# Kernel optimization log

Measured on AMD Instinct MI355X. Metric: run time of the kernel, lower is better.

The kernel has to match this reference:

```python
import jax, jax.numpy as jnp
import numpy as np

B, D, H, W, L = 32, 768, 14, 14, 77
TEMP_G, TEMP1, TEMP2, TEMP3 = 10.0, 4.0, 5.0, 10.0
LAMBDA_G, LAMBDA_L = 1.0, 1.0
EPS = 1e-8
NEG = -1e30


def setup_inputs() -> dict:
    key = jax.random.key(0)
    k1, k2, k3, k4, k5 = jax.random.split(key, 5)
    img_global = jax.random.normal(k1, (B, D), dtype=jnp.float32)
    img_local = jax.random.normal(k2, (B, D, H, W), dtype=jnp.float32)
    text_global = jax.random.normal(k3, (B, D), dtype=jnp.float32)
    text_local = jax.random.normal(k4, (B, L, D), dtype=jnp.float32)
    # ragged caption lengths: prefix attention mask, lengths in [10, L]
    lens = jax.random.randint(k5, (B,), 10, L + 1)
    attention_mask = (jnp.arange(L)[None, :] < lens[:, None]).astype(jnp.int32)
    return {"img_global": img_global, "img_local": img_local,
            "text_global": text_global, "text_local": text_local,
            "attention_mask": attention_mask}


def _ce_arange(scores):
    # cross entropy with labels = arange(n), mean reduction
    return jnp.mean(jax.nn.logsumexp(scores, axis=1) - jnp.diagonal(scores))


def _gloria_loss(img_global, img_local, text_global, text_local, attention_mask):
    mask = attention_mask.astype(bool)                      # [B, L]
    # ---- global contrastive loss ----
    in_ = img_global / jnp.maximum(jnp.linalg.norm(img_global, axis=1, keepdims=True), 1e-12)
    tn_ = text_global / jnp.maximum(jnp.linalg.norm(text_global, axis=1, keepdims=True), 1e-12)
    g_scores = (in_ @ tn_.T) * TEMP_G                       # [B, B]
    loss_global = 0.5 * (_ce_arange(g_scores) + _ce_arange(g_scores.T))

    # ---- local contrastive loss (vectorized over all text/image pairs) ----
    tl = jnp.swapaxes(text_local, 1, 2)                     # [B, D, L] (forward() transposes since L != D)
    ctx = img_local.reshape(B, D, H * W)                    # [B, D, S]
    # raw attention logits: text i words vs image j pixels -> [i, j, s, l]
    logits = jnp.einsum('jds,idl->ijsl', ctx, tl)
    logits = jnp.where(mask[:, None, None, :], logits, NEG)
    a1 = jax.nn.softmax(logits, axis=-1)                    # softmax over words (first softmax)
    a2 = jax.nn.softmax(TEMP1 * jnp.swapaxes(a1, 2, 3), axis=-1)  # [i, j, l, s], softmax over pixels
    wctx = jnp.einsum('jds,ijls->ijdl', ctx, a2)            # weighted context [i, j, D, l]
    # cosine similarity per word, over feature dim
    w12 = jnp.einsum('idl,ijdl->ijl', tl, wctx)
    n1 = jnp.linalg.norm(tl, axis=1)                        # [i, l]
    n2 = jnp.linalg.norm(wctx, axis=2)                      # [i, j, l]
    cos = w12 / jnp.maximum(n1[:, None, :] * n2, EPS)       # [i, j, l]
    row = jnp.exp(TEMP2 * cos) * mask[:, None, :]           # mask padded words
    sim = jnp.log(row.sum(axis=-1))                         # [i, j]  (local_agg='sum')
    # torch cats per-caption columns: similarities[j, i] -> transpose
    scores = sim.T * TEMP3                                  # [img j, text i]
    loss_local = 0.5 * (_ce_arange(scores) + _ce_arange(scores.T))

    return LAMBDA_G * loss_global + LAMBDA_L * loss_local


def reference(img_global, img_local, text_global, text_local, attention_mask):
    return _gloria_loss(img_global, img_local, text_global, text_local, attention_mask)
```

## Files before the change

### kernel.cpp

```cpp
#include <hip/hip_runtime.h>
#include <math.h>

#define NB 32
#define ND 768
#define NS 196
#define NL 77

typedef _Float16 f16x8 __attribute__((ext_vector_type(8)));
typedef float f32x4 __attribute__((ext_vector_type(4)));

__device__ __forceinline__ f32x4 mfma16(f16x8 a, f16x8 b, f32x4 c) {
  return __builtin_amdgcn_mfma_f32_16x16x32_f16(a, b, c, 0, 0, 0);
}

#define GLOAD16(gp, lp)                                          \
  __builtin_amdgcn_global_load_lds(                              \
      (const __attribute__((address_space(1))) void*)(gp),       \
      (__attribute__((address_space(3))) void*)(lp), 16, 0, 0)


__global__ __launch_bounds__(256) void prep_all_kernel(
    const float* __restrict__ text_local,
    const float* __restrict__ img_local,
    const int* __restrict__ amask,
    _Float16* __restrict__ txf, _Float16* __restrict__ cTf,
    float* __restrict__ n1ws, int* __restrict__ lenws) {
  const int bid = blockIdx.x;
  const int t = threadIdx.x;
  __shared__ float tile[32][213];

  if (bid < 960) {
    int tau = bid * 256 + t;
    int i = tau / 7680;
    int r = tau - i * 7680;
    int dk = r / 320;
    int r2 = r - dk * 320;
    int lt = r2 >> 6, lane = r2 & 63;
    int n16 = lane & 15, g = lane >> 4;
    int l = lt * 16 + n16;
    float v[8];
#pragma unroll
    for (int q = 0; q < 8; ++q) v[q] = 0.f;
    if (l < NL) {
      const float* src = text_local + ((size_t)i * NL + l) * ND + dk * 32 + g * 8;
      float4 a = *(const float4*)src;
      float4 b = *(const float4*)(src + 4);
      v[0] = a.x; v[1] = a.y; v[2] = a.z; v[3] = a.w;
      v[4] = b.x; v[5] = b.y; v[6] = b.z; v[7] = b.w;
    }
    f16x8 hv;
#pragma unroll
    for (int q = 0; q < 8; ++q) hv[q] = (_Float16)v[q];
    size_t base = (((size_t)i * 24 + dk) * 5 + lt) * 512 + (size_t)lane * 8;
    *(f16x8*)(txf + base) = hv;
  } else if (bid < 1344) {
    const int b2 = bid - 960;
    const int j = b2 / 12, dc = b2 - (b2 / 12) * 12;
    const float* src = img_local + ((size_t)j * ND + dc * 64) * NS;
#pragma unroll 1
    for (int h = 0; h < 2; ++h) {
      __syncthreads();
      for (int idx = t; idx < 1568; idx += 256) {
        int dd = idx / 49, sq = idx - dd * 49;
        float4 v = *(const float4*)(src + (size_t)(h * 32 + dd) * NS + sq * 4);
        tile[dd][sq * 4 + 0] = v.x;
        tile[dd][sq * 4 + 1] = v.y;
        tile[dd][sq * 4 + 2] = v.z;
        tile[dd][sq * 4 + 3] = v.w;
      }
      __syncthreads();
      const int dk = dc * 2 + h;
      for (int idx = t; idx < 832; idx += 256) {
        int lane = idx & 63;
        int S = idx >> 6;
        int n16 = lane & 15, g = lane >> 4;
        int s = S * 16 + n16;
        f16x8 hv;
#pragma unroll
        for (int e = 0; e < 8; ++e) {
          float v = (s < NS) ? tile[g * 8 + e][s] : 0.f;
          hv[e] = (_Float16)v;
        }
        size_t base = (((size_t)j * 13 + S) * 24 + dk) * 512 + (size_t)lane * 8;
        *(f16x8*)(cTf + base) = hv;
      }
    }
  } else {
    const int i = bid - 1344;
    const int lane = t & 63, w = t >> 6;
    __shared__ int slen;
    if (t == 0) slen = 0;
    __syncthreads();
    if (t < NL && amask[i * NL + t] != 0) atomicAdd(&slen, 1);
    for (int l = w; l < NL; l += 4) {
      const float4* p = (const float4*)(text_local + ((size_t)i * NL + l) * ND);
      float s = 0.f;
#pragma unroll
      for (int k = 0; k < 3; ++k) {
        float4 v = p[lane + 64 * k];
        s += v.x * v.x + v.y * v.y + v.z * v.z + v.w * v.w;
      }
#pragma unroll
      for (int off = 32; off; off >>= 1) s += __shfl_xor(s, off);
      if (lane == 0) n1ws[i * 80 + l] = sqrtf(s);
    }
    __syncthreads();
    if (t == 0) lenws[i] = slen;
  }
}

__global__ void mid_kernel(const _Float16* __restrict__ cTf, _Float16* __restrict__ Gf,
                           const float* __restrict__ img_global,
                           const float* __restrict__ text_global,
                           float* __restrict__ gscw,
                           const int* __restrict__ lenws, int* __restrict__ ordws) {
  const int bid = blockIdx.x;
  const int t = threadIdx.x;
  __shared__ __align__(16) float shi[ND];

  if (bid < 832) {
    const int j = bid / 26;
    const int rr = bid - j * 26;
    const int st = rr >> 1, ch = rr & 1;
    const int lane = t & 63, w = t >> 6;
    const int g = lane >> 4, n16 = lane & 15;
    const f32x4 z4 = {0.f, 0.f, 0.f, 0.f};
    f32x4 accG[2];
    accG[0] = z4; accG[1] = z4;
    const int base = ch * 7;
    const int ncols = ch ? 6 : 7;
    const size_t cj = (size_t)j * 13;
    for (int dk = 0; dk < 24; ++dk) {
      size_t ao = ((cj + st) * 24 + dk) * 512 + (size_t)lane * 8;
      f16x8 A = *(const f16x8*)(cTf + ao);
#pragma unroll
      for (int q = 0; q < 2; ++q) {
        int ntl = w + (q << 2);
        if (ntl < ncols) {
          int nt = base + ntl;
          size_t bo = ((cj + nt) * 24 + dk) * 512 + (size_t)lane * 8;
          f16x8 B = *(const f16x8*)(cTf + bo);
          accG[q] = mfma16(A, B, accG[q]);
        }
      }
    }
#pragma unroll
    for (int q = 0; q < 2; ++q) {
      int ntl = w + (q << 2);
      int nt = base + ntl;
      bool compute = (ntl < ncols);
      bool zfill = (ch == 1 && nt == 13);
      if (compute || zfill) {
#pragma unroll
        for (int r = 0; r < 4; ++r) {
          int col = nt * 16 + n16;
          float v = compute ? accG[q][r] : 0.f;
          int kt = col >> 5, gg = (col >> 3) & 3, e = col & 7;
          int lane2 = (g * 4 + r) + (gg << 4);
          size_t o = (((size_t)j * 13 + st) * 7 + kt) * 512 + (size_t)lane2 * 8 + e;
          Gf[o] = (_Float16)v;
        }
      }
    }
  } else if (bid < 864) {
    const int a = bid - 832;
    const int lane = t & 63, w = t >> 6;
    if (t < ND / 4) ((float4*)shi)[t] = ((const float4*)(img_global + (size_t)a * ND))[t];
    __syncthreads();
    for (int b = w; b < NB; b += 4) {
      const float4* pt = (const float4*)(text_global + (size_t)b * ND);
      const float4* pi = (const float4*)shi;
      float dot = 0.f, ni = 0.f, nt = 0.f;
#pragma unroll
      for (int k = 0; k < 3; ++k) {
        float4 x = pi[lane + 64 * k];
        float4 y = pt[lane + 64 * k];
        dot += x.x * y.x + x.y * y.y + x.z * y.z + x.w * y.w;
        ni  += x.x * x.x + x.y * x.y + x.z * x.z + x.w * x.w;
        nt  += y.x * y.x + y.y * y.y + y.z * y.z + y.w * y.w;
      }
#pragma unroll
      for (int off = 32; off; off >>= 1) {
        dot += __shfl_xor(dot, off);
        ni  += __shfl_xor(ni, off);
        nt  += __shfl_xor(nt, off);
      }
      if (lane == 0)
        gscw[a * NB + b] = dot / fmaxf(sqrtf(ni), 1e-12f) / fmaxf(sqrtf(nt), 1e-12f) * 10.0f;
    }
  } else {
    if (t == 0) {
      int o[32];
      for (int k = 0; k < 32; ++k) o[k] = k;
      for (int x = 0; x < 31; ++x) {
        int best = x;
        for (int y = x + 1; y < 32; ++y)
          if (lenws[o[y]] > lenws[o[best]]) best = y;
        int tmp = o[x]; o[x] = o[best]; o[best] = tmp;
      }
      for (int k = 0; k < 32; ++k) ordws[k] = o[k];
    }
  }
}

__global__ __launch_bounds__(512, 3) void pair_kernel(
    const _Float16* __restrict__ txf, const _Float16* __restrict__ cTf,
    const _Float16* __restrict__ Gf,
    const float* __restrict__ n1ws, const int* __restrict__ lenws,
    const int* __restrict__ ordws,
    float* __restrict__ simws) {
  const int t = threadIdx.x;
  const int wg = ((blockIdx.x & 7) << 6) + (blockIdx.x >> 3);
  const int j = wg >> 4;
  const int m = wg & 15;
  const int i0 = ordws[m], i1 = ordws[31 - m];
  const int len0 = lenws[i0], len1 = lenws[i1];
  const int nlt0 = (len0 + 15) >> 4, nlt1 = (len1 + 15) >> 4;
  const int lane = t & 63, wid = t >> 6;
  const int g = lane >> 4, n16 = lane & 15;
  const bool vb = (wid < 5);

  __shared__ __align__(16) union {
    _Float16 e2f[7 * 5 * 64 * 8];
    _Float16 b1[2][2][5][512];
  } U;
  __shared__ float w12s[80], z2s[80], n2s[80];

  const f32x4 z4 = {0.f, 0.f, 0.f, 0.f};
  f32x4 acc[2][2][5];
#pragma unroll
  for (int p = 0; p < 2; ++p)
#pragma unroll
    for (int q = 0; q < 2; ++q)
#pragma unroll
      for (int lt = 0; lt < 5; ++lt) acc[p][q][lt] = z4;

  const _Float16* txi0 = txf + (size_t)i0 * 24 * 5 * 512;
  const _Float16* txi1 = txf + (size_t)i1 * 24 * 5 * 512;
  const size_t cj = (size_t)j * 13;
  const int c0 = (wid < 5) ? wid : (wid - 5);

  GLOAD16(txi0 + ((size_t)c0 << 9) + ((size_t)lane << 3), &U.b1[0][0][c0][0]);
  GLOAD16(txi1 + ((size_t)c0 << 9) + ((size_t)lane << 3), &U.b1[0][1][c0][0]);
  __syncthreads();

#pragma unroll 1
  for (int dk = 0; dk < 24; ++dk) {
    const int cur = dk & 1;
    f16x8 Aa, Ab;
    {
      size_t ao = ((cj + wid) * 24 + dk) * 512 + ((size_t)lane << 3);
      Aa = *(const f16x8*)(cTf + ao);
    }
    if (vb) {
      size_t ao = ((cj + wid + 8) * 24 + dk) * 512 + ((size_t)lane << 3);
      Ab = *(const f16x8*)(cTf + ao);
    }
    if (dk < 23) {
      GLOAD16(txi0 + ((size_t)((dk + 1) * 5 + c0) << 9) + ((size_t)lane << 3),
              &U.b1[cur ^ 1][0][c0][0]);
      GLOAD16(txi1 + ((size_t)((dk + 1) * 5 + c0) << 9) + ((size_t)lane << 3),
              &U.b1[cur ^ 1][1][c0][0]);
    }
    __builtin_amdgcn_s_setprio(1);
#pragma unroll
    for (int lt = 0; lt < 5; ++lt) {
      if (lt < nlt0) {
        f16x8 B0 = *(const f16x8*)&U.b1[cur][0][lt][lane << 3];
        acc[0][0][lt] = mfma16(Aa, B0, acc[0][0][lt]);
        if (vb) acc[0][1][lt] = mfma16(Ab, B0, acc[0][1][lt]);
      }
      if (lt < nlt1) {
        f16x8 B1 = *(const f16x8*)&U.b1[cur][1][lt][lane << 3];
        acc[1][0][lt] = mfma16(Aa, B1, acc[1][0][lt]);
        if (vb) acc[1][1][lt] = mfma16(Ab, B1, acc[1][1][lt]);
      }
    }
    __builtin_amdgcn_s_setprio(0);
    __syncthreads();
  }

#pragma unroll
  for (int p = 0; p < 2; ++p) {
    const int ip   = p ? i1 : i0;
    const int lenp = p ? len1 : len0;
    const int nltp = p ? nlt1 : nlt0;

    __syncthreads();
    if (t < 80) { w12s[t] = 0.f; z2s[t] = 0.f; n2s[t] = 0.f; }
    for (int idx = t; idx < 2240; idx += 512)
      ((uint4*)U.e2f)[idx] = make_uint4(0, 0, 0, 0);
    __syncthreads();

    float w12loc[5], z2loc[5];
#pragma unroll
    for (int lt = 0; lt < 5; ++lt) { w12loc[lt] = 0.f; z2loc[lt] = 0.f; }
#pragma unroll
    for (int q = 0; q < 2; ++q) {
      const int S = wid + (q << 3);
      if (q == 0 || vb) {
#pragma unroll
        for (int r = 0; r < 4; ++r) {
          int s = S * 16 + g * 4 + r;
          bool srow = (s < NS);
          float mx = -1e30f;
#pragma unroll
          for (int lt = 0; lt < 5; ++lt) {
            if (lt < nltp) {
              if ((lt * 16 + n16) < lenp) mx = fmaxf(mx, acc[p][q][lt][r]);
            }
          }
          mx = fmaxf(mx, __shfl_xor(mx, 1));
          mx = fmaxf(mx, __shfl_xor(mx, 2));
          mx = fmaxf(mx, __shfl_xor(mx, 4));
          mx = fmaxf(mx, __shfl_xor(mx, 8));
          float z = 0.f;
          float ev[5];
#pragma unroll
          for (int lt = 0; lt < 5; ++lt) {
            float e = 0.f;
            if (lt < nltp) {
              if ((lt * 16 + n16) < lenp) e = __expf(acc[p][q][lt][r] - mx);
            }
            ev[lt] = e;
            z += e;
          }
          z += __shfl_xor(z, 1);
          z += __shfl_xor(z, 2);
          z += __shfl_xor(z, 4);
          z += __shfl_xor(z, 8);
          float inv = 4.0f / z;
#pragma unroll
          for (int lt = 0; lt < 5; ++lt) {
            if (lt < nltp) {
              if (((lt * 16 + n16) < lenp) && srow) {
                float e2 = __expf(ev[lt] * inv);
                w12loc[lt] += e2 * acc[p][q][lt][r];
                z2loc[lt] += e2;
                int kt = s >> 5, kk = s & 31;
                U.e2f[(((kt * 5) + lt) * 64 + (n16 + ((kk >> 3) << 4))) * 8 + (kk & 7)] = (_Float16)e2;
              }
            }
          }
        }
      }
    }
#pragma unroll
    for (int lt = 0; lt < 5; ++lt) {
      w12loc[lt] += __shfl_xor(w12loc[lt], 16);
      w12loc[lt] += __shfl_xor(w12loc[lt], 32);
      z2loc[lt] += __shfl_xor(z2loc[lt], 16);
      z2loc[lt] += __shfl_xor(z2loc[lt], 32);
    }
    if (lane < 16) {
#pragma unroll
      for (int lt = 0; lt < 5; ++lt) {
        if (lt < nltp) {
          atomicAdd(&w12s[lt * 16 + lane], w12loc[lt]);
          atomicAdd(&z2s[lt * 16 + lane], z2loc[lt]);
        }
      }
    }
    __syncthreads();

    float n2loc[5];
#pragma unroll
    for (int lt = 0; lt < 5; ++lt) n2loc[lt] = 0.f;
#pragma unroll
    for (int q = 0; q < 2; ++q) {
      const int S = wid + (q << 3);
      if (q == 0 || vb) {
        f32x4 a2[5];
#pragma unroll
        for (int lt = 0; lt < 5; ++lt) a2[lt] = z4;
        const _Float16* gp = Gf + (((size_t)j * 13 + S) * 7) * 512 + ((size_t)lane << 3);
        f16x8 GA = *(const f16x8*)gp;
#pragma unroll
        for (int kt = 0; kt < 7; ++kt) {
          f16x8 GAN;
          if (kt < 6) GAN = *(const f16x8*)(gp + (size_t)(kt + 1) * 512);
          __builtin_amdgcn_s_setprio(1);
#pragma unroll
          for (int lt = 0; lt < 5; ++lt) {
            if (lt < nltp) {
              f16x8 Bv = *(const f16x8*)&U.e2f[(((kt * 5) + lt) * 64 + lane) * 8];
              a2[lt] = mfma16(GA, Bv, a2[lt]);
            }
          }
          __builtin_amdgcn_s_setprio(0);
          if (kt < 6) GA = GAN;
        }
#pragma unroll
        for (int lt = 0; lt < 5; ++lt) {
          if (lt < nltp) {
#pragma unroll
            for (int r = 0; r < 4; ++r) {
              int s = S * 16 + g * 4 + r;
              int kt = s >> 5, kk = s & 31;
              float e2v = (float)U.e2f[(((kt * 5) + lt) * 64 + (n16 + ((kk >> 3) << 4))) * 8 + (kk & 7)];
              n2loc[lt] += e2v * a2[lt][r];
            }
          }
        }
      }
    }
#pragma unroll
    for (int lt = 0; lt < 5; ++lt) {
      n2loc[lt] += __shfl_xor(n2loc[lt], 16);
      n2loc[lt] += __shfl_xor(n2loc[lt], 32);
    }
    if (lane < 16) {
#pragma unroll
      for (int lt = 0; lt < 5; ++lt) {
        if (lt < nltp) atomicAdd(&n2s[lt * 16 + lane], n2loc[lt]);
      }
    }
    __syncthreads();

    if (t < lenp) {
      float z2 = z2s[t];
      float w12v = w12s[t] / z2;
      float n2v = sqrtf(n2s[t]) / z2;
      float n1v = n1ws[ip * 80 + t];
      float cosv = w12v / fmaxf(n1v * n2v, 1e-8f);
      w12s[t] = __expf(5.0f * cosv);
    }
    __syncthreads();
    if (wid == 0) {
      float e = (lane < lenp) ? w12s[lane] : 0.f;
      if (lane + 64 < lenp) e += w12s[lane + 64];
      e += __shfl_xor(e, 1);
      e += __shfl_xor(e, 2);
      e += __shfl_xor(e, 4);
      e += __shfl_xor(e, 8);
      e += __shfl_xor(e, 16);
      e += __shfl_xor(e, 32);
      if (lane == 0) simws[ip * NB + j] = __logf(e);
    }
  }
}

__global__ void loss_kernel(const float* __restrict__ gscw,
                            const float* __restrict__ simws,
                            float* __restrict__ out) {
  const int t = threadIdx.x;
  __shared__ float gs[NB][NB];
  __shared__ float sl[NB][NB];
  __shared__ float parts[4][NB];
  {
    float4 gv = ((const float4*)gscw)[t];
    ((float4*)gs)[t] = gv;
    float4 v = ((const float4*)simws)[t];
    int ii = t >> 3;
    int j0 = (t & 7) * 4;
    sl[j0 + 0][ii] = v.x * 10.0f;
    sl[j0 + 1][ii] = v.y * 10.0f;
    sl[j0 + 2][ii] = v.z * 10.0f;
    sl[j0 + 3][ii] = v.w * 10.0f;
  }
  __syncthreads();
  if (t < NB) {
    float m, z;
    m = -1e30f;
    for (int c = 0; c < NB; ++c) m = fmaxf(m, gs[t][c]);
    z = 0.f;
    for (int c = 0; c < NB; ++c) z += __expf(gs[t][c] - m);
    parts[0][t] = m + __logf(z) - gs[t][t];

    m = -1e30f;
    for (int c = 0; c < NB; ++c) m = fmaxf(m, gs[c][t]);
    z = 0.f;
    for (int c = 0; c < NB; ++c) z += __expf(gs[c][t] - m);
    parts[1][t] = m + __logf(z) - gs[t][t];

    m = -1e30f;
    for (int c = 0; c < NB; ++c) m = fmaxf(m, sl[t][c]);
    z = 0.f;
    for (int c = 0; c < NB; ++c) z += __expf(sl[t][c] - m);
    parts[2][t] = m + __logf(z) - sl[t][t];

    m = -1e30f;
    for (int c = 0; c < NB; ++c) m = fmaxf(m, sl[c][t]);
    z = 0.f;
    for (int c = 0; c < NB; ++c) z += __expf(sl[c][t] - m);
    parts[3][t] = m + __logf(z) - sl[t][t];
  }
  __syncthreads();
  if (t == 0) {
    float s0 = 0.f, s1 = 0.f, s2 = 0.f, s3 = 0.f;
    for (int r = 0; r < NB; ++r) {
      s0 += parts[0][r]; s1 += parts[1][r];
      s2 += parts[2][r]; s3 += parts[3][r];
    }
    out[0] = 0.5f * (s0 + s1) / 32.0f + 0.5f * (s2 + s3) / 32.0f;
  }
}

extern "C" void kernel_launch(void* const* d_in, const int* in_sizes, int n_in,
                              void* d_out, int out_size, void* d_ws, size_t ws_size,
                              hipStream_t stream) {
  (void)in_sizes; (void)n_in; (void)out_size; (void)ws_size;
  const float* img_global  = (const float*)d_in[0];
  const float* img_local   = (const float*)d_in[1];
  const float* text_global = (const float*)d_in[2];
  const float* text_local  = (const float*)d_in[3];
  const int*   amask       = (const int*)d_in[4];

  _Float16* txf = (_Float16*)d_ws;
  _Float16* cTf = txf + (size_t)1966080;
  _Float16* Gf  = cTf + (size_t)5111808;
  float* fsm  = (float*)(Gf + (size_t)1490944);
  float* n1ws  = fsm;
  float* simws = fsm + 2560;
  float* gscw  = fsm + 3584;
  int*   lenws = (int*)(fsm + 4608);
  int*   ordws = (int*)(fsm + 4640);

  prep_all_kernel<<<1376, 256, 0, stream>>>(text_local, img_local, amask,
                                            txf, cTf, n1ws, lenws);
  mid_kernel<<<865, 256, 0, stream>>>(cTf, Gf, img_global, text_global,
                                      gscw, lenws, ordws);
  pair_kernel<<<512, 512, 0, stream>>>(txf, cTf, Gf, n1ws, lenws, ordws, simws);
  loss_kernel<<<1, 256, 0, stream>>>(gscw, simws, (float*)d_out);
}
```

Measured before the change: 121.9 us.

## Triple-chunk the pair-kernel K loop and fuse the loss kernel via last-block counter

The pair kernel's reduction loop now handles three K-chunks per iteration, loading three A fragments and prefetching three B tiles into a larger LDS double buffer. This cuts barriers and loop overhead by a factor of three. The separate single-block loss kernel is removed: each pair block bumps a global counter after writing its similarity, and the last block to finish computes the cross-entropy loss. This saves one kernel launch but uses more LDS, which may lower occupancy, and relies on atomic and fence ordering for correctness.

```diff
diff --git a/kernel.cpp b/kernel.cpp
--- a/kernel.cpp
+++ b/kernel.cpp
@@ -113,7 +113,8 @@
                            const float* __restrict__ img_global,
                            const float* __restrict__ text_global,
                            float* __restrict__ gscw,
-                           const int* __restrict__ lenws, int* __restrict__ ordws) {
+                           const int* __restrict__ lenws, int* __restrict__ ordws,
+                           unsigned int* __restrict__ donews) {
   const int bid = blockIdx.x;
   const int t = threadIdx.x;
   __shared__ __align__(16) float shi[ND];
@@ -199,6 +200,7 @@
         int tmp = o[x]; o[x] = o[best]; o[best] = tmp;
       }
       for (int k = 0; k < 32; ++k) ordws[k] = o[k];
+      *donews = 0u;
     }
   }
 }
@@ -208,7 +210,8 @@
     const _Float16* __restrict__ Gf,
     const float* __restrict__ n1ws, const int* __restrict__ lenws,
     const int* __restrict__ ordws,
-    float* __restrict__ simws) {
+    float* __restrict__ simws, const float* __restrict__ gscw,
+    unsigned int* __restrict__ donews, float* __restrict__ out) {
   const int t = threadIdx.x;
   const int wg = ((blockIdx.x & 7) << 6) + (blockIdx.x >> 3);
   const int j = wg >> 4;
@@ -222,9 +225,11 @@
 
   __shared__ __align__(16) union {
     _Float16 e2f[7 * 5 * 64 * 8];
-    _Float16 b1[2][2][5][512];
+    _Float16 b1[2][3][2][5][512];
+    struct { float gs[NB][NB]; float sl[NB][NB]; float parts[4][NB]; } loss;
   } U;
   __shared__ float w12s[80], z2s[80], n2s[80];
+  __shared__ int amLast;
 
   const f32x4 z4 = {0.f, 0.f, 0.f, 0.f};
   f32x4 acc[2][2][5];
@@ -240,40 +245,56 @@
   const size_t cj = (size_t)j * 13;
   const int c0 = (wid < 5) ? wid : (wid - 5);
 
-  GLOAD16(txi0 + ((size_t)c0 << 9) + ((size_t)lane << 3), &U.b1[0][0][c0][0]);
-  GLOAD16(txi1 + ((size_t)c0 << 9) + ((size_t)lane << 3), &U.b1[0][1][c0][0]);
+#pragma unroll
+  for (int d = 0; d < 3; ++d) {
+    GLOAD16(txi0 + ((size_t)(d * 5 + c0) << 9) + ((size_t)lane << 3), &U.b1[0][d][0][c0][0]);
+    GLOAD16(txi1 + ((size_t)(d * 5 + c0) << 9) + ((size_t)lane << 3), &U.b1[0][d][1][c0][0]);
+  }
   __syncthreads();
 
 #pragma unroll 1
-  for (int dk = 0; dk < 24; ++dk) {
-    const int cur = dk & 1;
-    f16x8 Aa, Ab;
+  for (int dkp = 0; dkp < 8; ++dkp) {
+    const int cur = dkp & 1;
+    const int dk0 = dkp * 3;
+    f16x8 Aa0, Aa1, Aa2, Ab0, Ab1, Ab2;
     {
-      size_t ao = ((cj + wid) * 24 + dk) * 512 + ((size_t)lane << 3);
-      Aa = *(const f16x8*)(cTf + ao);
+      size_t ao = ((cj + wid) * 24 + dk0) * 512 + ((size_t)lane << 3);
+      Aa0 = *(const f16x8*)(cTf + ao);
+      Aa1 = *(const f16x8*)(cTf + ao + 512);
+      Aa2 = *(const f16x8*)(cTf + ao + 1024);
     }
     if (vb) {
-      size_t ao = ((cj + wid + 8) * 24 + dk) * 512 + ((size_t)lane << 3);
-      Ab = *(const f16x8*)(cTf + ao);
-    }
-    if (dk < 23) {
-      GLOAD16(txi0 + ((size_t)((dk + 1) * 5 + c0) << 9) + ((size_t)lane << 3),
-              &U.b1[cur ^ 1][0][c0][0]);
-      GLOAD16(txi1 + ((size_t)((dk + 1) * 5 + c0) << 9) + ((size_t)lane << 3),
-              &U.b1[cur ^ 1][1][c0][0]);
+      size_t ao = ((cj + wid + 8) * 24 + dk0) * 512 + ((size_t)lane << 3);
+      Ab0 = *(const f16x8*)(cTf + ao);
+      Ab1 = *(const f16x8*)(cTf + ao + 512);
+      Ab2 = *(const f16x8*)(cTf + ao + 1024);
+    }
+    if (dkp < 7) {
+#pragma unroll
+      for (int d = 0; d < 3; ++d) {
+        GLOAD16(txi0 + ((size_t)((dk0 + 3 + d) * 5 + c0) << 9) + ((size_t)lane << 3),
+                &U.b1[cur ^ 1][d][0][c0][0]);
+        GLOAD16(txi1 + ((size_t)((dk0 + 3 + d) * 5 + c0) << 9) + ((size_t)lane << 3),
+                &U.b1[cur ^ 1][d][1][c0][0]);
+      }
     }
     __builtin_amdgcn_s_setprio(1);
 #pragma unroll
-    for (int lt = 0; lt < 5; ++lt) {
-      if (lt < nlt0) {
-        f16x8 B0 = *(const f16x8*)&U.b1[cur][0][lt][lane << 3];
-        acc[0][0][lt] = mfma16(Aa, B0, acc[0][0][lt]);
-        if (vb) acc[0][1][lt] = mfma16(Ab, B0, acc[0][1][lt]);
-      }
-      if (lt < nlt1) {
-        f16x8 B1 = *(const f16x8*)&U.b1[cur][1][lt][lane << 3];
-        acc[1][0][lt] = mfma16(Aa, B1, acc[1][0][lt]);
-        if (vb) acc[1][1][lt] = mfma16(Ab, B1, acc[1][1][lt]);
+    for (int d = 0; d < 3; ++d) {
+      f16x8 Aa = (d == 0) ? Aa0 : (d == 1) ? Aa1 : Aa2;
+      f16x8 Ab = (d == 0) ? Ab0 : (d == 1) ? Ab1 : Ab2;
+#pragma unroll
+      for (int lt = 0; lt < 5; ++lt) {
+        if (lt < nlt0) {
+          f16x8 B0 = *(const f16x8*)&U.b1[cur][d][0][lt][lane << 3];
+          acc[0][0][lt] = mfma16(Aa, B0, acc[0][0][lt]);
+          if (vb) acc[0][1][lt] = mfma16(Ab, B0, acc[0][1][lt]);
+        }
+        if (lt < nlt1) {
+          f16x8 B1 = *(const f16x8*)&U.b1[cur][d][1][lt][lane << 3];
+          acc[1][0][lt] = mfma16(Aa, B1, acc[1][0][lt]);
+          if (vb) acc[1][1][lt] = mfma16(Ab, B1, acc[1][1][lt]);
+        }
       }
     }
     __builtin_amdgcn_s_setprio(0);
@@ -435,62 +456,61 @@
       e += __shfl_xor(e, 8);
       e += __shfl_xor(e, 16);
       e += __shfl_xor(e, 32);
-      if (lane == 0) simws[ip * NB + j] = __logf(e);
-    }
-  }
-}
-
-__global__ void loss_kernel(const float* __restrict__ gscw,
-                            const float* __restrict__ simws,
-                            float* __restrict__ out) {
-  const int t = threadIdx.x;
-  __shared__ float gs[NB][NB];
-  __shared__ float sl[NB][NB];
-  __shared__ float parts[4][NB];
-  {
+      if (lane == 0) atomicExch(&simws[ip * NB + j], __logf(e));
+    }
+  }
+
+  __syncthreads();
+  if (t == 0) {
+    __threadfence();
+    unsigned int old = atomicAdd(donews, 1u);
+    amLast = (old == 511u) ? 1 : 0;
+  }
+  __syncthreads();
+  if (!amLast) return;
+
+  if (t < 256) {
     float4 gv = ((const float4*)gscw)[t];
-    ((float4*)gs)[t] = gv;
-    float4 v = ((const float4*)simws)[t];
-    int ii = t >> 3;
-    int j0 = (t & 7) * 4;
-    sl[j0 + 0][ii] = v.x * 10.0f;
-    sl[j0 + 1][ii] = v.y * 10.0f;
-    sl[j0 + 2][ii] = v.z * 10.0f;
-    sl[j0 + 3][ii] = v.w * 10.0f;
+    *(float4*)&U.loss.gs[t >> 3][(t & 7) * 4] = gv;
+    for (int k = t; k < 1024; k += 256) {
+      int ii = k >> 5, jj = k & 31;
+      float v = atomicAdd(&simws[k], 0.0f);
+      U.loss.sl[jj][ii] = v * 10.0f;
+    }
   }
   __syncthreads();
   if (t < NB) {
-    float m, z;
-    m = -1e30f;
-    for (int c = 0; c < NB; ++c) m = fmaxf(m, gs[t][c]);
+    float mx, z;
+    mx = -1e30f;
+    for (int c = 0; c < NB; ++c) mx = fmaxf(mx, U.loss.gs[t][c]);
     z = 0.f;
-    for (int c = 0; c < NB; ++c) z += __expf(gs[t][c] - m);
-    parts[0][t] = m + __logf(z) - gs[t][t];
-
-    m = -1e30f;
-    for (int c = 0; c < NB; ++c) m = fmaxf(m, gs[c][t]);
+    for (int c = 0; c < NB; ++c) z += __expf(U.loss.gs[t][c] - mx);
+    U.loss.parts[0][t] = mx + __logf(z) - U.loss.gs[t][t];
+
+    mx = -1e30f;
+    for (int c = 0; c < NB; ++c) mx = fmaxf(mx, U.loss.gs[c][t]);
     z = 0.f;
-    for (int c = 0; c < NB; ++c) z += __expf(gs[c][t] - m);
-    parts[1][t] = m + __logf(z) - gs[t][t];
-
-    m = -1e30f;
-    for (int c = 0; c < NB; ++c) m = fmaxf(m, sl[t][c]);
+    for (int c = 0; c < NB; ++c) z += __expf(U.loss.gs[c][t] - mx);
+    U.loss.parts[1][t] = mx + __logf(z) - U.loss.gs[t][t];
+
+    mx = -1e30f;
+    for (int c = 0; c < NB; ++c) mx = fmaxf(mx, U.loss.sl[t][c]);
     z = 0.f;
-    for (int c = 0; c < NB; ++c) z += __expf(sl[t][c] - m);
-    parts[2][t] = m + __logf(z) - sl[t][t];
-
-    m = -1e30f;
-    for (int c = 0; c < NB; ++c) m = fmaxf(m, sl[c][t]);
+    for (int c = 0; c < NB; ++c) z += __expf(U.loss.sl[t][c] - mx);
+    U.loss.parts[2][t] = mx + __logf(z) - U.loss.sl[t][t];
+
+    mx = -1e30f;
+    for (int c = 0; c < NB; ++c) mx = fmaxf(mx, U.loss.sl[c][t]);
     z = 0.f;
-    for (int c = 0; c < NB; ++c) z += __expf(sl[c][t] - m);
-    parts[3][t] = m + __logf(z) - sl[t][t];
+    for (int c = 0; c < NB; ++c) z += __expf(U.loss.sl[c][t] - mx);
+    U.loss.parts[3][t] = mx + __logf(z) - U.loss.sl[t][t];
   }
   __syncthreads();
   if (t == 0) {
     float s0 = 0.f, s1 = 0.f, s2 = 0.f, s3 = 0.f;
     for (int r = 0; r < NB; ++r) {
-      s0 += parts[0][r]; s1 += parts[1][r];
-      s2 += parts[2][r]; s3 += parts[3][r];
+      s0 += U.loss.parts[0][r]; s1 += U.loss.parts[1][r];
+      s2 += U.loss.parts[2][r]; s3 += U.loss.parts[3][r];
     }
     out[0] = 0.5f * (s0 + s1) / 32.0f + 0.5f * (s2 + s3) / 32.0f;
   }
@@ -515,11 +535,12 @@
   float* gscw  = fsm + 3584;
   int*   lenws = (int*)(fsm + 4608);
   int*   ordws = (int*)(fsm + 4640);
+  unsigned int* donews = (unsigned int*)(fsm + 4672);
 
   prep_all_kernel<<<1376, 256, 0, stream>>>(text_local, img_local, amask,
                                             txf, cTf, n1ws, lenws);
   mid_kernel<<<865, 256, 0, stream>>>(cTf, Gf, img_global, text_global,
-                                      gscw, lenws, ordws);
-  pair_kernel<<<512, 512, 0, stream>>>(txf, cTf, Gf, n1ws, lenws, ordws, simws);
-  loss_kernel<<<1, 256, 0, stream>>>(gscw, simws, (float*)d_out);
+                                      gscw, lenws, ordws, donews);
+  pair_kernel<<<512, 512, 0, stream>>>(txf, cTf, Gf, n1ws, lenws, ordws,
+                                       simws, gscw, donews, (float*)d_out);
 }
```

After: 122.9 us. About the same (+0.8%).
